# Kernel tuning notes

Measured on AMD Instinct MI355X. Metric: run time of the kernel, lower is better.

## Reference

```python
import jax, jax.numpy as jnp
import numpy as np

D_MODEL = 1024
NHEAD = 16
HEAD_DIM = D_MODEL // NHEAD
FF = 4096
ALPHA = 1.4142135  # deepnorm_alpha
WIN = (127, 128)   # sliding window (left, right)
EPS = 1e-5
ROPE_BASE = 10000.0


def rmsnorm(x, g):
    ms = jnp.mean(x * x, axis=-1, keepdims=True)
    return x * jax.lax.rsqrt(ms + EPS) * g


def rope(x):
    # x: [B, T, H, D]; non-interleaved rotary over full head dim
    T, D = x.shape[1], x.shape[-1]
    half = D // 2
    inv_freq = 1.0 / (ROPE_BASE ** (jnp.arange(half, dtype=jnp.float32) * 2.0 / D))
    ang = jnp.arange(T, dtype=jnp.float32)[:, None] * inv_freq[None, :]  # [T, half]
    cos = jnp.cos(ang)[None, :, None, :]
    sin = jnp.sin(ang)[None, :, None, :]
    x1, x2 = x[..., :half], x[..., half:]
    return jnp.concatenate([x1 * cos - x2 * sin, x2 * cos + x1 * sin], axis=-1)


def setup_inputs() -> dict:
    key = jax.random.key(0)
    ks = jax.random.split(key, 8)
    d, h = D_MODEL, FF
    return {
        "x": jax.random.normal(ks[0], (2, 2048, d), jnp.float32),
        "Wqkv": jax.random.normal(ks[1], (3 * d, d), jnp.float32) * 0.02,
        "Wout": jax.random.normal(ks[2], (d, d), jnp.float32) * 0.02,
        "bout": jnp.zeros((d,), jnp.float32),
        "W1": jax.random.normal(ks[3], (2 * h, d), jnp.float32) * 0.02,
        "W2": jax.random.normal(ks[4], (d, h), jnp.float32) * 0.02,
        "g1": jnp.ones((d,), jnp.float32),
        "g2": jnp.ones((d,), jnp.float32),
    }


def reference(x, Wqkv, Wout, bout, W1, W2, g1, g2):
    B, T, d = x.shape
    # --- self attention with RoPE + sliding window band mask ---
    qkv = (x @ Wqkv.T).reshape(B, T, 3, NHEAD, HEAD_DIM)
    q, k, v = qkv[:, :, 0], qkv[:, :, 1], qkv[:, :, 2]  # [B,T,H,Dh]
    q = rope(q)
    k = rope(k)
    q = jnp.swapaxes(q, 1, 2)  # [B,H,T,Dh]
    k = jnp.swapaxes(k, 1, 2)
    v = jnp.swapaxes(v, 1, 2)
    scale = 1.0 / np.sqrt(HEAD_DIM)
    scores = jnp.einsum('bhqd,bhkd->bhqk', q, k) * scale
    idx = jnp.arange(T)
    rel = idx[None, :] - idx[:, None]  # j - i
    band = (rel >= -WIN[0]) & (rel <= WIN[1])  # [T,T] allowed positions
    scores = jnp.where(band[None, None], scores, -jnp.inf)
    attn = jax.nn.softmax(scores, axis=-1)
    o = jnp.einsum('bhqk,bhkd->bhqd', attn, v)
    o = jnp.swapaxes(o, 1, 2).reshape(B, T, d)
    a = o @ Wout.T + bout
    # --- deepnorm residual 1 + RMSNorm ---
    x1 = a + ALPHA * x
    x2 = rmsnorm(x1, g1)
    # --- SwiGLU MLP: y, gate = fc1(x).chunk(2); y*gate*sigmoid(gate) ---
    yg = x2 @ W1.T
    y, gate = jnp.split(yg, 2, axis=-1)
    y = y * gate * jax.nn.sigmoid(gate)
    y = y @ W2.T
    # --- deepnorm residual 2 + RMSNorm ---
    x3 = y + ALPHA * x2
    return rmsnorm(x3, g2)
```

## Files before the change

### kernel.cpp

```cpp
#include <hip/hip_runtime.h>

#define T_SEQ   2048
#define NHEADS  16
#define DHEAD   64
#define DMODEL  1024
#define ALPHA_C 1.4142135f
#define EPS_C   1e-5f

typedef __attribute__((ext_vector_type(8))) short bf16x8;
typedef __attribute__((ext_vector_type(4))) short bf16x4;
typedef __attribute__((ext_vector_type(4))) float floatx4;

__device__ __forceinline__ float bf2f(unsigned short u) {
  union { unsigned int i; float f; } v;
  v.i = ((unsigned int)u) << 16;
  return v.f;
}
__device__ __forceinline__ unsigned short f2bf(float f) {
  union { float f; unsigned int i; } v;
  v.f = f;
  unsigned int u = v.i;
  u += 0x7FFF + ((u >> 16) & 1);
  return (unsigned short)(u >> 16);
}

__device__ __forceinline__ void gload_lds16(const void* g, void* l) {
  __builtin_amdgcn_global_load_lds(
      (const __attribute__((address_space(1))) void*)g,
      (__attribute__((address_space(3))) void*)l, 16, 0, 0);
}

__global__ void convert_all(const float* __restrict__ Wqkv,
                            const float* __restrict__ Wout,
                            const float* __restrict__ W1,
                            const float* __restrict__ W2,
                            const float* __restrict__ x,
                            unsigned short* __restrict__ ws)
{
  size_t i = ((size_t)blockIdx.x * 256 + threadIdx.x) * 8;
  const float* src;
  size_t off;
  if      (i <  3145728) { src = Wqkv; off = i; }
  else if (i <  4194304) { src = Wout; off = i -  3145728; }
  else if (i < 12582912) { src = W1;   off = i -  4194304; }
  else if (i < 16777216) { src = W2;   off = i - 12582912; }
  else                   { src = x;    off = i - 16777216; }
  floatx4 a = *(const floatx4*)(src + off);
  floatx4 b = *(const floatx4*)(src + off + 4);
  bf16x8 o;
  #pragma unroll
  for (int u = 0; u < 4; u++) {
    o[u]     = (short)f2bf(a[u]);
    o[4 + u] = (short)f2bf(b[u]);
  }
  *(bf16x8*)(ws + i) = o;
}

__global__ void build_rope_lut(float* __restrict__ cosT,
                               float* __restrict__ sinT)
{
  int gid = blockIdx.x * 256 + threadIdx.x;
  int t = gid >> 5, i = gid & 31;
  float fr = powf(10000.f, -(float)i * (1.f / 32.f));
  float sn, cs;
  sincosf((float)t * fr, &sn, &cs);
  cosT[gid] = cs;
  sinT[gid] = sn;
}

template<int BN>
__global__ __launch_bounds__(256) void gemm_lds(
    const unsigned short* __restrict__ A,
    const unsigned short* __restrict__ W,
    unsigned short* __restrict__ C,
    const float* __restrict__ bias,
    int M, int N, int K, int lda)
{
  constexpr int WN = BN / 2;
  constexpr int NJ = WN / 16;
  __shared__ unsigned short As[128 * 32];
  __shared__ unsigned short Bs[BN * 32];

  const int tid  = threadIdx.x;
  const int lane = tid & 63;
  const int wave = tid >> 6;
  const int wm = (wave >> 1) * 64;
  const int wn = (wave & 1) * WN;
  const int mBase = blockIdx.y * 128;
  const int nBase = blockIdx.x * BN;

  const int sRow = lane >> 2;
  const int sCol = (lane & 3) * 8;

  floatx4 acc[4][NJ];
  #pragma unroll
  for (int i = 0; i < 4; i++)
    #pragma unroll
    for (int j = 0; j < NJ; j++) acc[i][j] = (floatx4){0.f, 0.f, 0.f, 0.f};

  const int mrow = lane & 15;
  const int kq   = (lane >> 4) * 8;

  for (int kb = 0; kb < K; kb += 32) {
    __syncthreads();
    #pragma unroll
    for (int j = 0; j < 2; j++) {
      int r = wave * 32 + j * 16 + sRow;
      gload_lds16(A + (size_t)(mBase + r) * lda + kb + sCol,
                  &As[wave * 1024 + j * 512 + lane * 8]);
    }
    if constexpr (BN == 128) {
      #pragma unroll
      for (int j = 0; j < 2; j++) {
        int r = wave * 32 + j * 16 + sRow;
        gload_lds16(W + (size_t)(nBase + r) * K + kb + sCol,
                    &Bs[wave * 1024 + j * 512 + lane * 8]);
      }
    } else {
      int r = wave * 16 + sRow;
      gload_lds16(W + (size_t)(nBase + r) * K + kb + sCol,
                  &Bs[wave * 512 + lane * 8]);
    }
    __syncthreads();

    bf16x8 af[4], bfr[NJ];
    #pragma unroll
    for (int i = 0; i < 4; i++)
      af[i] = *(const bf16x8*)&As[(wm + i * 16 + mrow) * 32 + kq];
    #pragma unroll
    for (int j = 0; j < NJ; j++)
      bfr[j] = *(const bf16x8*)&Bs[(wn + j * 16 + mrow) * 32 + kq];
    #pragma unroll
    for (int i = 0; i < 4; i++)
      #pragma unroll
      for (int j = 0; j < NJ; j++)
        acc[i][j] = __builtin_amdgcn_mfma_f32_16x16x32_bf16(af[i], bfr[j], acc[i][j], 0, 0, 0);
  }

  const int col0 = lane & 15;
  const int row0 = (lane >> 4) * 4;
  #pragma unroll
  for (int j = 0; j < NJ; j++) {
    const int col = nBase + wn + j * 16 + col0;
    const float badd = bias ? bias[col] : 0.f;
    #pragma unroll
    for (int i = 0; i < 4; i++) {
      #pragma unroll
      for (int r = 0; r < 4; r++) {
        const int row = mBase + wm + i * 16 + row0 + r;
        C[(size_t)row * N + col] = f2bf(acc[i][j][r] + badd);
      }
    }
  }
}

__global__ __launch_bounds__(256) void gemm_w2_splitk(
    const unsigned short* __restrict__ A,
    const unsigned short* __restrict__ W,
    float* __restrict__ Cp)
{
  __shared__ unsigned short As[128 * 32];
  __shared__ unsigned short Bs[64 * 32];

  const int tid  = threadIdx.x;
  const int lane = tid & 63;
  const int wave = tid >> 6;
  const int wm = (wave >> 1) * 64;
  const int wn = (wave & 1) * 32;
  const int mBase = blockIdx.y * 128;
  const int nBase = blockIdx.x * 64;
  const int kOff  = blockIdx.z * 2048;

  const int sRow = lane >> 2;
  const int sCol = (lane & 3) * 8;

  floatx4 acc[4][2];
  #pragma unroll
  for (int i = 0; i < 4; i++)
    #pragma unroll
    for (int j = 0; j < 2; j++) acc[i][j] = (floatx4){0.f, 0.f, 0.f, 0.f};

  const int mrow = lane & 15;
  const int kq   = (lane >> 4) * 8;

  for (int kb = 0; kb < 2048; kb += 32) {
    __syncthreads();
    #pragma unroll
    for (int j = 0; j < 2; j++) {
      int r = wave * 32 + j * 16 + sRow;
      gload_lds16(A + (size_t)(mBase + r) * 4096 + kOff + kb + sCol,
                  &As[wave * 1024 + j * 512 + lane * 8]);
    }
    {
      int r = wave * 16 + sRow;
      gload_lds16(W + (size_t)(nBase + r) * 4096 + kOff + kb + sCol,
                  &Bs[wave * 512 + lane * 8]);
    }
    __syncthreads();

    bf16x8 af[4], bfr[2];
    #pragma unroll
    for (int i = 0; i < 4; i++)
      af[i] = *(const bf16x8*)&As[(wm + i * 16 + mrow) * 32 + kq];
    #pragma unroll
    for (int j = 0; j < 2; j++)
      bfr[j] = *(const bf16x8*)&Bs[(wn + j * 16 + mrow) * 32 + kq];
    #pragma unroll
    for (int i = 0; i < 4; i++)
      #pragma unroll
      for (int j = 0; j < 2; j++)
        acc[i][j] = __builtin_amdgcn_mfma_f32_16x16x32_bf16(af[i], bfr[j], acc[i][j], 0, 0, 0);
  }

  const int col0 = lane & 15;
  const int row0 = (lane >> 4) * 4;
  float* dst = Cp + (size_t)blockIdx.z * 4096 * 1024;
  #pragma unroll
  for (int j = 0; j < 2; j++) {
    const int col = nBase + wn + j * 16 + col0;
    #pragma unroll
    for (int i = 0; i < 4; i++)
      #pragma unroll
      for (int r = 0; r < 4; r++) {
        const int row = mBase + wm + i * 16 + row0 + r;
        dst[(size_t)row * 1024 + col] = acc[i][j][r];
      }
  }
}

__global__ __launch_bounds__(256) void gemm_qkv_rope(
    const unsigned short* __restrict__ A,
    const unsigned short* __restrict__ W,
    const float* __restrict__ cosT,
    const float* __restrict__ sinT,
    unsigned short* __restrict__ Qd,
    unsigned short* __restrict__ Kd,
    unsigned short* __restrict__ Vd)
{
  constexpr int K = 1024;
  __shared__ unsigned short As[128 * 32];
  __shared__ unsigned short Bs[128 * 32];

  const int tid  = threadIdx.x;
  const int lane = tid & 63;
  const int wave = tid >> 6;
  const int wm = (wave >> 1) * 64;
  const int wn = (wave & 1) * 64;
  const int mBase = blockIdx.y * 128;
  const int nBase = blockIdx.x * 128;

  const int sRow = lane >> 2;
  const int sCol = (lane & 3) * 8;

  floatx4 acc[4][4];
  #pragma unroll
  for (int i = 0; i < 4; i++)
    #pragma unroll
    for (int j = 0; j < 4; j++) acc[i][j] = (floatx4){0.f, 0.f, 0.f, 0.f};

  const int mrow = lane & 15;
  const int kq   = (lane >> 4) * 8;

  for (int kb = 0; kb < K; kb += 32) {
    __syncthreads();
    #pragma unroll
    for (int j = 0; j < 2; j++) {
      int r = wave * 32 + j * 16 + sRow;
      gload_lds16(A + (size_t)(mBase + r) * K + kb + sCol,
                  &As[wave * 1024 + j * 512 + lane * 8]);
      gload_lds16(W + (size_t)(nBase + r) * K + kb + sCol,
                  &Bs[wave * 1024 + j * 512 + lane * 8]);
    }
    __syncthreads();

    bf16x8 af[4], bfr[4];
    #pragma unroll
    for (int i = 0; i < 4; i++) {
      af[i]  = *(const bf16x8*)&As[(wm + i * 16 + mrow) * 32 + kq];
      bfr[i] = *(const bf16x8*)&Bs[(wn + i * 16 + mrow) * 32 + kq];
    }
    #pragma unroll
    for (int i = 0; i < 4; i++)
      #pragma unroll
      for (int j = 0; j < 4; j++)
        acc[i][j] = __builtin_amdgcn_mfma_f32_16x16x32_bf16(af[i], bfr[j], acc[i][j], 0, 0, 0);
  }

  const int col0 = lane & 15;
  const int row0 = (lane >> 4) * 4;
  const int colBase = nBase + wn;
  const int sect = colBase >> 10;
  const int h    = (colBase & 1023) >> 6;
  unsigned short* dst = (sect == 0) ? Qd : (sect == 1) ? Kd : Vd;

  if (sect < 2) {
    #pragma unroll
    for (int it = 0; it < 4; it++) {
      #pragma unroll
      for (int r = 0; r < 4; r++) {
        const int row = mBase + wm + it * 16 + row0 + r;
        const int b = row >> 11, t = row & 2047;
        size_t ob = ((size_t)((b * NHEADS + h) * T_SEQ + t)) * DHEAD;
        const int tb = t * 32;
        float c0 = cosT[tb + col0],      s0 = sinT[tb + col0];
        float c1 = cosT[tb + col0 + 16], s1 = sinT[tb + col0 + 16];
        float x1a = acc[it][0][r], x2a = acc[it][2][r];
        float x1b = acc[it][1][r], x2b = acc[it][3][r];
        dst[ob + col0]      = f2bf(x1a * c0 - x2a * s0);
        dst[ob + col0 + 32] = f2bf(x2a * c0 + x1a * s0);
        dst[ob + col0 + 16] = f2bf(x1b * c1 - x2b * s1);
        dst[ob + col0 + 48] = f2bf(x2b * c1 + x1b * s1);
      }
    }
  } else {
    #pragma unroll
    for (int it = 0; it < 4; it++)
      #pragma unroll
      for (int j = 0; j < 4; j++)
        #pragma unroll
        for (int r = 0; r < 4; r++) {
          const int row = mBase + wm + it * 16 + row0 + r;
          const int b = row >> 11, t = row & 2047;
          dst[((size_t)((b * NHEADS + h) * T_SEQ + t)) * DHEAD + j * 16 + col0] =
              f2bf(acc[it][j][r]);
        }
  }
}

#define BAR() __builtin_amdgcn_s_barrier()
#define LGKM0() do { asm volatile("s_waitcnt lgkmcnt(0)" ::: "memory"); \
                     __builtin_amdgcn_sched_barrier(0); } while (0)

#define RD_A(bb, mh)                                                      \
  _Pragma("unroll") for (int i = 0; i < 4; i++)                           \
  _Pragma("unroll") for (int s = 0; s < 2; s++)                           \
    af[i][s] = *(const bf16x8*)&lds[(bb) + aRd +                          \
        ((mh) * 64 + i * 16 + mrow) * 64 + (kq0 ^ (s << 5))];

#define RD_B(bb, nh)                                                      \
  _Pragma("unroll") for (int n = 0; n < 2; n++)                           \
  _Pragma("unroll") for (int s = 0; s < 2; s++)                           \
    bf[(nh) * 2 + n][s] = *(const bf16x8*)&lds[(bb) + bRd +               \
        (bRow0 + ((nh) * 2 + n) * 16 + mrow) * 64 + (kq0 ^ (s << 5))];

#define MFMA16(mh, nh)                                                    \
  _Pragma("unroll") for (int i = 0; i < 4; i++)                           \
  _Pragma("unroll") for (int n = 0; n < 2; n++)                           \
  _Pragma("unroll") for (int s = 0; s < 2; s++)                           \
    acc[(mh) * 4 + i][(nh) * 2 + n] =                                     \
        __builtin_amdgcn_mfma_f32_16x16x32_bf16(                          \
            af[i][s], bf[(nh) * 2 + n][s],                                \
            acc[(mh) * 4 + i][(nh) * 2 + n], 0, 0, 0);

__global__ __launch_bounds__(512, 2) void gemm_w1_swiglu_8ph(
    const unsigned short* __restrict__ A,
    const unsigned short* __restrict__ W1,
    unsigned short* __restrict__ ys)
{
  __shared__ unsigned short lds[65536];

  const int tid  = threadIdx.x;
  const int lane = tid & 63;
  const int wid  = tid >> 6;
  const int wr   = wid >> 2;
  const int wc   = wid & 3;
  const int mrow = lane & 15;
  const int quad = lane >> 4;
  const int kq0  = (quad ^ (mrow & 7)) * 8;

  const int bid  = blockIdx.y * 32 + blockIdx.x;
  const int c8   = bid & 7;
  const int u    = bid >> 3;
  const int mBase = ((c8 >> 2) * 8 + (u >> 3)) * 256;
  const int nBase = ((c8 &  3) * 8 + (u &  7)) * 128;

  const int r0 = tid >> 3;
  const int ce = (((tid & 7) ^ (r0 & 7)) * 8);
  const size_t aoff0 = (size_t)(mBase + r0) * 1024 + ce;
  const size_t aoff1 = aoff0 + (size_t)64 * 1024;
  auto growf = [&](int br) {
    int col = nBase + (br >> 6) * 32 + (br & 31);
    return ((br >> 5) & 1) ? 4096 + col : col;
  };
  const size_t boff00 = (size_t)growf(r0)       * 1024 + ce;
  const size_t boff01 = (size_t)growf(64 + r0)  * 1024 + ce;
  const size_t boff10 = (size_t)growf(128 + r0) * 1024 + ce;
  const size_t boff11 = (size_t)growf(192 + r0) * 1024 + ce;
  const int d0 = tid * 8;

  auto stA = [&](int buf, int h, int kt) {
    const unsigned short* g = A + (size_t)kt * 64 + (h ? (size_t)128 * 1024 : 0);
    int base = buf * 32768 + h * 8192;
    gload_lds16(g + aoff0, &lds[base + d0]);
    gload_lds16(g + aoff1, &lds[base + 4096 + d0]);
  };
  auto stB = [&](int buf, int h, int kt) {
    const unsigned short* g = W1 + (size_t)kt * 64;
    int base = buf * 32768 + 16384 + h * 8192;
    gload_lds16(g + (h ? boff10 : boff00), &lds[base + d0]);
    gload_lds16(g + (h ? boff11 : boff01), &lds[base + 4096 + d0]);
  };

  floatx4 acc[8][4];
  #pragma unroll
  for (int i = 0; i < 8; i++)
    #pragma unroll
    for (int n = 0; n < 4; n++) acc[i][n] = (floatx4){0.f, 0.f, 0.f, 0.f};
  bf16x8 af[4][2], bf[4][2];

  const int aRd   = wr * 8192;
  const int bRd   = 16384 + (wc >> 1) * 8192;
  const int bRow0 = (wc & 1) * 64;

  stB(0, 0, 0); stA(0, 0, 0); stA(0, 1, 0); stB(0, 1, 0);
  stB(1, 0, 1); stA(1, 0, 1);
  asm volatile("s_waitcnt vmcnt(4)" ::: "memory");
  BAR();

  for (int t = 0; t < 16; ++t) {
    const int cur = t & 1;
    const int nxt = cur ^ 1;
    const int bb  = cur * 32768;
    const int ta  = (t + 1 < 16) ? t + 1 : 15;
    const int tb  = (t + 2 < 16) ? t + 2 : 15;

    RD_A(bb, 0); RD_B(bb, 0);
    stA(nxt, 1, ta);
    BAR(); LGKM0();
    __builtin_amdgcn_s_setprio(1);
    MFMA16(0, 0);
    __builtin_amdgcn_s_setprio(0);
    BAR();

    RD_B(bb, 1);
    stB(nxt, 1, ta);
    BAR(); LGKM0();
    __builtin_amdgcn_s_setprio(1);
    MFMA16(0, 1);
    __builtin_amdgcn_s_setprio(0);
    BAR();

    RD_A(bb, 1);
    stB(cur, 0, tb);
    BAR(); LGKM0();
    __builtin_amdgcn_s_setprio(1);
    MFMA16(1, 1);
    __builtin_amdgcn_s_setprio(0);
    BAR();

    stA(cur, 0, tb);
    BAR(); LGKM0();
    __builtin_amdgcn_s_setprio(1);
    MFMA16(1, 0);
    __builtin_amdgcn_s_setprio(0);
    asm volatile("s_waitcnt vmcnt(4)" ::: "memory");
    BAR();
  }

  const int col0 = lane & 15;
  const int row0 = (lane >> 4) * 4;
  #pragma unroll
  for (int n = 0; n < 2; n++) {
    const int col = nBase + wc * 32 + n * 16 + col0;
    #pragma unroll
    for (int i = 0; i < 8; i++) {
      const int rowb = mBase + wr * 128 + i * 16 + row0;
      #pragma unroll
      for (int r = 0; r < 4; r++) {
        float y = acc[i][n][r], g = acc[i][n + 2][r];
        float sig = 1.f / (1.f + __expf(-g));
        ys[(size_t)(rowb + r) * 4096 + col] = f2bf(y * g * sig);
      }
    }
  }
  asm volatile("s_waitcnt vmcnt(0)" ::: "memory");
}

__global__ __launch_bounds__(256) void attn_mfma(
    const unsigned short* __restrict__ Qg,
    const unsigned short* __restrict__ Kg,
    const unsigned short* __restrict__ Vg,
    unsigned short* __restrict__ Og)
{
  __shared__ unsigned short KV[23040];
  __shared__ unsigned short Qs[64 * 72];
  __shared__ unsigned short Ps[4 * 16 * 328];

  const int tid  = threadIdx.x;
  const int lane = tid & 63;
  const int wave = tid >> 6;
  const int c    = lane & 15;
  const int quad = lane >> 4;
  const int blk  = blockIdx.x;
  const int bh   = blk >> 5;
  const int qBase = (blk & 31) * 64;
  const size_t hbase = (size_t)bh * T_SEQ * DHEAD;

  for (int e = tid; e < 320 * 8; e += 256) {
    int row = e >> 3, ch = e & 7;
    int kg = qBase - 127 + row;
    int kgc = min(max(kg, 0), T_SEQ - 1);
    *(bf16x8*)&KV[row * 72 + ch * 8] =
        *(const bf16x8*)(Kg + hbase + (size_t)kgc * DHEAD + ch * 8);
  }
  for (int e = tid; e < 64 * 8; e += 256) {
    int row = e >> 3, ch = e & 7;
    *(bf16x8*)&Qs[row * 72 + ch * 8] =
        *(const bf16x8*)(Qg + hbase + (size_t)(qBase + row) * DHEAD + ch * 8);
  }
  __syncthreads();

  bf16x8 aq[2];
  #pragma unroll
  for (int hh = 0; hh < 2; hh++)
    aq[hh] = *(const bf16x8*)&Qs[(wave * 16 + c) * 72 + hh * 32 + quad * 8];

  floatx4 s[20];
  #pragma unroll
  for (int kt = 0; kt < 20; kt++) {
    bf16x8 b0 = *(const bf16x8*)&KV[(kt * 16 + c) * 72 + quad * 8];
    bf16x8 b1 = *(const bf16x8*)&KV[(kt * 16 + c) * 72 + 32 + quad * 8];
    floatx4 t = (floatx4){0.f, 0.f, 0.f, 0.f};
    t = __builtin_amdgcn_mfma_f32_16x16x32_bf16(aq[0], b0, t, 0, 0, 0);
    t = __builtin_amdgcn_mfma_f32_16x16x32_bf16(aq[1], b1, t, 0, 0, 0);
    s[kt] = t;
  }
  __syncthreads();

  for (int ch = wave; ch < 5; ch += 4) {
    int koff = ch * 64 + lane;
    int kg = qBase - 127 + koff;
    int kgc = min(max(kg, 0), T_SEQ - 1);
    const unsigned short* vrow = Vg + hbase + (size_t)kgc * DHEAD;
    #pragma unroll
    for (int dg = 0; dg < 8; dg++) {
      bf16x8 v8 = *(const bf16x8*)(vrow + dg * 8);
      #pragma unroll
      for (int j = 0; j < 8; j++)
        KV[(dg * 8 + j) * 328 + koff] = (unsigned short)v8[j];
    }
  }

  const int kLoMin = max(0, 127 - qBase);
  const int kHiMax = min(319, 2047 + 127 - qBase);
  float mx[4] = {-3e38f, -3e38f, -3e38f, -3e38f};
  #pragma unroll
  for (int kt = 0; kt < 20; kt++) {
    const int koff = kt * 16 + c;
    #pragma unroll
    for (int reg = 0; reg < 4; reg++) {
      const int qrow = wave * 16 + quad * 4 + reg;
      const int d = koff - qrow;
      bool ok = (d >= 0) && (d <= 255) && (koff >= kLoMin) && (koff <= kHiMax);
      float val = ok ? s[kt][reg] * 0.125f : -3e38f;
      s[kt][reg] = val;
      mx[reg] = fmaxf(mx[reg], val);
    }
  }
  #pragma unroll
  for (int reg = 0; reg < 4; reg++)
    #pragma unroll
    for (int m = 1; m <= 8; m <<= 1)
      mx[reg] = fmaxf(mx[reg], __shfl_xor(mx[reg], m));

  float ls[4] = {0.f, 0.f, 0.f, 0.f};
  #pragma unroll
  for (int kt = 0; kt < 20; kt++) {
    const int koff = kt * 16 + c;
    #pragma unroll
    for (int reg = 0; reg < 4; reg++) {
      float p = __expf(s[kt][reg] - mx[reg]);
      ls[reg] += p;
      Ps[wave * 5248 + (quad * 4 + reg) * 328 + koff] = f2bf(p);
    }
  }
  float inv[4];
  #pragma unroll
  for (int reg = 0; reg < 4; reg++) {
    #pragma unroll
    for (int m = 1; m <= 8; m <<= 1) ls[reg] += __shfl_xor(ls[reg], m);
    inv[reg] = 1.f / ls[reg];
  }
  __syncthreads();

  floatx4 oacc[4];
  #pragma unroll
  for (int nt = 0; nt < 4; nt++) oacc[nt] = (floatx4){0.f, 0.f, 0.f, 0.f};
  #pragma unroll
  for (int kt2 = 0; kt2 < 10; kt2++) {
    bf16x8 a = *(const bf16x8*)&Ps[wave * 5248 + c * 328 + kt2 * 32 + quad * 8];
    #pragma unroll
    for (int nt = 0; nt < 4; nt++) {
      bf16x8 bb = *(const bf16x8*)&KV[(nt * 16 + c) * 328 + kt2 * 32 + quad * 8];
      oacc[nt] = __builtin_amdgcn_mfma_f32_16x16x32_bf16(a, bb, oacc[nt], 0, 0, 0);
    }
  }

  const int b = bh >> 4, h = bh & 15;
  #pragma unroll
  for (int nt = 0; nt < 4; nt++) {
    #pragma unroll
    for (int reg = 0; reg < 4; reg++) {
      const int qg = qBase + wave * 16 + quad * 4 + reg;
      Og[((size_t)(b * T_SEQ + qg)) * DMODEL + h * DHEAD + nt * 16 + c] =
          f2bf(oacc[nt][reg] * inv[reg]);
    }
  }
}

__global__ __launch_bounds__(256) void rmsnorm_mid(
    const unsigned short* __restrict__ a,
    const float* __restrict__ x,
    const float* __restrict__ g,
    unsigned short* __restrict__ out)
{
  __shared__ float red[4];
  const int row = blockIdx.x;
  const int tid = threadIdx.x;
  const size_t base = (size_t)row * DMODEL;
  const int c = tid * 4;
  bf16x4  av = *(const bf16x4*)(a + base + c);
  floatx4 xv = *(const floatx4*)(x + base + c);
  floatx4 gv = *(const floatx4*)(g + c);
  float s[4], ss = 0.f;
  #pragma unroll
  for (int j = 0; j < 4; j++) {
    s[j] = bf2f((unsigned short)av[j]) + ALPHA_C * xv[j];
    ss += s[j] * s[j];
  }
  #pragma unroll
  for (int m = 1; m <= 32; m <<= 1) ss += __shfl_xor(ss, m);
  if ((tid & 63) == 0) red[tid >> 6] = ss;
  __syncthreads();
  float ms = (red[0] + red[1] + red[2] + red[3]) * (1.f / DMODEL);
  float scl = rsqrtf(ms + EPS_C);
  bf16x4 ov;
  #pragma unroll
  for (int j = 0; j < 4; j++) ov[j] = (short)f2bf(s[j] * scl * gv[j]);
  *(bf16x4*)(out + base + c) = ov;
}

__global__ __launch_bounds__(256) void rmsnorm_final_sk(
    const float* __restrict__ p0,
    const float* __restrict__ p1,
    const unsigned short* __restrict__ x2,
    const float* __restrict__ g,
    float* __restrict__ out)
{
  __shared__ float red[4];
  const int row = blockIdx.x;
  const int tid = threadIdx.x;
  const size_t base = (size_t)row * DMODEL;
  const int c = tid * 4;
  floatx4 a0 = *(const floatx4*)(p0 + base + c);
  floatx4 a1 = *(const floatx4*)(p1 + base + c);
  bf16x4  xv = *(const bf16x4*)(x2 + base + c);
  floatx4 gv = *(const floatx4*)(g + c);
  float s[4], ss = 0.f;
  #pragma unroll
  for (int j = 0; j < 4; j++) {
    s[j] = (a0[j] + a1[j]) + ALPHA_C * bf2f((unsigned short)xv[j]);
    ss += s[j] * s[j];
  }
  #pragma unroll
  for (int m = 1; m <= 32; m <<= 1) ss += __shfl_xor(ss, m);
  if ((tid & 63) == 0) red[tid >> 6] = ss;
  __syncthreads();
  float ms = (red[0] + red[1] + red[2] + red[3]) * (1.f / DMODEL);
  float scl = rsqrtf(ms + EPS_C);
  floatx4 ov;
  #pragma unroll
  for (int j = 0; j < 4; j++) ov[j] = s[j] * scl * gv[j];
  *(floatx4*)(out + base + c) = ov;
}

extern "C" void kernel_launch(void* const* d_in, const int* in_sizes, int n_in,
                              void* d_out, int out_size, void* d_ws, size_t ws_size,
                              hipStream_t stream) {
  (void)in_sizes; (void)n_in; (void)out_size; (void)ws_size;
  const float* x    = (const float*)d_in[0];
  const float* Wqkv = (const float*)d_in[1];
  const float* Wout = (const float*)d_in[2];
  const float* bout = (const float*)d_in[3];
  const float* W1   = (const float*)d_in[4];
  const float* W2   = (const float*)d_in[5];
  const float* g1   = (const float*)d_in[6];
  const float* g2   = (const float*)d_in[7];
  float* out = (float*)d_out;

  unsigned short* ws    = (unsigned short*)d_ws;
  unsigned short* Wqkvb = ws;
  unsigned short* Woutb = ws + 3145728;
  unsigned short* W1b   = ws + 4194304;
  unsigned short* W2b   = ws + 12582912;
  unsigned short* P1    = ws + 16777216;
  unsigned short* x2    = ws + 20971520;
  unsigned short* q     = ws + 25165824;
  unsigned short* k     = ws + 29360128;
  unsigned short* v     = ws + 33554432;
  unsigned short* o     = ws + 37748736;
  unsigned short* ys    = ws + 25165824;
  float* cosT = (float*)(ws + 37748736);
  float* sinT = cosT + 65536;
  float* p0   = (float*)(ws + 41943040);
  float* p1   = (float*)(ws + 50331648);

  build_rope_lut<<<256, 256, 0, stream>>>(cosT, sinT);
  convert_all<<<10240, 256, 0, stream>>>(Wqkv, Wout, W1, W2, x, ws);
  gemm_qkv_rope<<<dim3(24, 32), 256, 0, stream>>>(P1, Wqkvb, cosT, sinT, q, k, v);
  attn_mfma<<<32 * (T_SEQ / 64), 256, 0, stream>>>(q, k, v, o);
  gemm_lds<64><<<dim3(16, 32), 256, 0, stream>>>(o, Woutb, P1, bout, 4096, 1024, 1024, 1024);
  rmsnorm_mid<<<4096, 256, 0, stream>>>(P1, x, g1, x2);
  gemm_w1_swiglu_8ph<<<dim3(32, 16), 512, 0, stream>>>(x2, W1b, ys);
  gemm_w2_splitk<<<dim3(16, 32, 2), 256, 0, stream>>>(ys, W2b, p0);
  rmsnorm_final_sk<<<4096, 256, 0, stream>>>(p0, p1, x2, g2, out);
}
```

Before: 384.0 us.

## Restructure W1 SwiGLU GEMM phases to overlap LDS reads with MFMA

Reworks the 4-phase main loop of the W1+SwiGLU GEMM. All B fragments are now read once per k-tile instead of twice, and LDS reads are split by k-half so MFMAs on the first half start after a partial lgkmcnt wait while the second half is still loading. Barriers drop from two per phase to one, moved to the start of each phase. The aim is to hide LDS latency and cut sync overhead, at the cost of more live fragment registers and a more delicate ordering between barriers and the async global-to-LDS writes.

```diff
diff --git a/kernel.cpp b/kernel.cpp
--- a/kernel.cpp
+++ b/kernel.cpp
@@ -328,28 +328,24 @@
 }
 
 #define BAR() __builtin_amdgcn_s_barrier()
-#define LGKM0() do { asm volatile("s_waitcnt lgkmcnt(0)" ::: "memory"); \
-                     __builtin_amdgcn_sched_barrier(0); } while (0)
-
-#define RD_A(bb, mh)                                                      \
+#define SCB() __builtin_amdgcn_sched_barrier(0)
+
+#define RD_A_S(bb, mh, s)                                                 \
   _Pragma("unroll") for (int i = 0; i < 4; i++)                           \
-  _Pragma("unroll") for (int s = 0; s < 2; s++)                           \
     af[i][s] = *(const bf16x8*)&lds[(bb) + aRd +                          \
-        ((mh) * 64 + i * 16 + mrow) * 64 + (kq0 ^ (s << 5))];
-
-#define RD_B(bb, nh)                                                      \
-  _Pragma("unroll") for (int n = 0; n < 2; n++)                           \
-  _Pragma("unroll") for (int s = 0; s < 2; s++)                           \
-    bf[(nh) * 2 + n][s] = *(const bf16x8*)&lds[(bb) + bRd +               \
-        (bRow0 + ((nh) * 2 + n) * 16 + mrow) * 64 + (kq0 ^ (s << 5))];
-
-#define MFMA16(mh, nh)                                                    \
+        ((mh) * 64 + i * 16 + mrow) * 64 + (kq0 ^ ((s) << 5))];
+
+#define RD_B_S(bb, s)                                                     \
+  _Pragma("unroll") for (int n = 0; n < 4; n++)                           \
+    bfr[n][s] = *(const bf16x8*)&lds[(bb) + bRd +                         \
+        (bRow0 + n * 16 + mrow) * 64 + (kq0 ^ ((s) << 5))];
+
+#define MFMA8(mh, nh, s)                                                  \
   _Pragma("unroll") for (int i = 0; i < 4; i++)                           \
   _Pragma("unroll") for (int n = 0; n < 2; n++)                           \
-  _Pragma("unroll") for (int s = 0; s < 2; s++)                           \
     acc[(mh) * 4 + i][(nh) * 2 + n] =                                     \
         __builtin_amdgcn_mfma_f32_16x16x32_bf16(                          \
-            af[i][s], bf[(nh) * 2 + n][s],                                \
+            af[i][s], bfr[(nh) * 2 + n][s],                               \
             acc[(mh) * 4 + i][(nh) * 2 + n], 0, 0, 0);
 
 __global__ __launch_bounds__(512, 2) void gemm_w1_swiglu_8ph(
@@ -406,7 +402,7 @@
   for (int i = 0; i < 8; i++)
     #pragma unroll
     for (int n = 0; n < 4; n++) acc[i][n] = (floatx4){0.f, 0.f, 0.f, 0.f};
-  bf16x8 af[4][2], bf[4][2];
+  bf16x8 af[4][2], bfr[4][2];
 
   const int aRd   = wr * 8192;
   const int bRd   = 16384 + (wc >> 1) * 8192;
@@ -415,7 +411,6 @@
   stB(0, 0, 0); stA(0, 0, 0); stA(0, 1, 0); stB(0, 1, 0);
   stB(1, 0, 1); stA(1, 0, 1);
   asm volatile("s_waitcnt vmcnt(4)" ::: "memory");
-  BAR();
 
   for (int t = 0; t < 16; ++t) {
     const int cur = t & 1;
@@ -424,37 +419,50 @@
     const int ta  = (t + 1 < 16) ? t + 1 : 15;
     const int tb  = (t + 2 < 16) ? t + 2 : 15;
 
-    RD_A(bb, 0); RD_B(bb, 0);
+    BAR();
     stA(nxt, 1, ta);
-    BAR(); LGKM0();
+    RD_A_S(bb, 0, 0); RD_B_S(bb, 0);
+    SCB();
+    RD_A_S(bb, 0, 1); RD_B_S(bb, 1);
+    asm volatile("s_waitcnt lgkmcnt(8)" ::: "memory");
+    SCB();
     __builtin_amdgcn_s_setprio(1);
-    MFMA16(0, 0);
+    MFMA8(0, 0, 0);
     __builtin_amdgcn_s_setprio(0);
+    asm volatile("s_waitcnt lgkmcnt(0)" ::: "memory");
+    SCB();
+    __builtin_amdgcn_s_setprio(1);
+    MFMA8(0, 0, 1);
+    __builtin_amdgcn_s_setprio(0);
+
     BAR();
-
-    RD_B(bb, 1);
     stB(nxt, 1, ta);
-    BAR(); LGKM0();
     __builtin_amdgcn_s_setprio(1);
-    MFMA16(0, 1);
+    MFMA8(0, 1, 0); MFMA8(0, 1, 1);
     __builtin_amdgcn_s_setprio(0);
+
     BAR();
-
-    RD_A(bb, 1);
     stB(cur, 0, tb);
-    BAR(); LGKM0();
+    RD_A_S(bb, 1, 0);
+    SCB();
+    RD_A_S(bb, 1, 1);
+    asm volatile("s_waitcnt lgkmcnt(4)" ::: "memory");
+    SCB();
     __builtin_amdgcn_s_setprio(1);
-    MFMA16(1, 1);
+    MFMA8(1, 1, 0);
     __builtin_amdgcn_s_setprio(0);
+    asm volatile("s_waitcnt lgkmcnt(0)" ::: "memory");
+    SCB();
+    __builtin_amdgcn_s_setprio(1);
+    MFMA8(1, 1, 1);
+    __builtin_amdgcn_s_setprio(0);
+
     BAR();
-
     stA(cur, 0, tb);
-    BAR(); LGKM0();
     __builtin_amdgcn_s_setprio(1);
-    MFMA16(1, 0);
+    MFMA8(1, 0, 0); MFMA8(1, 0, 1);
     __builtin_amdgcn_s_setprio(0);
     asm volatile("s_waitcnt vmcnt(4)" ::: "memory");
-    BAR();
   }
 
   const int col0 = lane & 15;
```

New measurement: 383.1 us. Within noise of the previous version (-0.2%).
